# Kernel tuning notes

Measured on AMD Instinct MI355X. Metric: run time of the kernel, lower is better.

The kernel has to match this reference:

```python
import jax, jax.numpy as jnp
import numpy as np

B, S, D, H = 4, 2048, 1024, 4096
EPS = 1e-5

def _layernorm(x, g, b):
    mu = jnp.mean(x, axis=-1, keepdims=True)
    var = jnp.mean(jnp.square(x - mu), axis=-1, keepdims=True)
    return (x - mu) * jax.lax.rsqrt(var + EPS) * g + b

def setup_inputs() -> dict:
    key = jax.random.key(0)
    ks = jax.random.split(key, 8)
    s = lambda d: 1.0 / np.sqrt(d)
    return {
        "x": jax.random.normal(ks[0], (B, S, D), jnp.float32),
        "Wq": jax.random.normal(ks[1], (D, D), jnp.float32) * s(D),
        "bq": jnp.zeros((D,), jnp.float32),
        "Wk": jax.random.normal(ks[2], (D, D), jnp.float32) * s(D),
        "bk": jnp.zeros((D,), jnp.float32),
        "Wv": jax.random.normal(ks[3], (D, D), jnp.float32) * s(D),
        "bv": jnp.zeros((D,), jnp.float32),
        "Wo": jax.random.normal(ks[4], (D, D), jnp.float32) * s(D),
        "bo": jnp.zeros((D,), jnp.float32),
        "g1": jnp.ones((D,), jnp.float32),
        "be1": jnp.zeros((D,), jnp.float32),
        "g2": jnp.ones((D,), jnp.float32),
        "be2": jnp.zeros((D,), jnp.float32),
        "W1": jax.random.normal(ks[5], (D, H), jnp.float32) * s(D),
        "b1": jnp.zeros((H,), jnp.float32),
        "W2": jax.random.normal(ks[6], (H, D), jnp.float32) * s(H),
        "b2": jnp.zeros((D,), jnp.float32),
    }

def reference(x, Wq, bq, Wk, bk, Wv, bv, Wo, bo, g1, be1, g2, be2, W1, b1, W2, b2):
    # pre-norm self-attention + residual
    xn = _layernorm(x, g1, be1)
    q = xn @ Wq + bq            # [B,S,D]
    k = xn @ Wk + bk
    v = xn @ Wv + bv
    scale = 1.0 / jnp.sqrt(jnp.float32(D))
    scores = jnp.einsum("bsd,btd->bst", q, k) * scale  # [B,S,S]
    attn = jax.nn.softmax(scores, axis=-1)
    attn_out = jnp.einsum("bst,btd->bsd", attn, v) @ Wo + bo
    x = x + attn_out
    # pre-norm MLP + residual
    xn2 = _layernorm(x, g2, be2)
    ffn = jax.nn.relu(xn2 @ W1 + b1) @ W2 + b2
    out = x + ffn
    return out, attn
```

## Files before the change

kernel.cpp:

```cpp
#include <hip/hip_runtime.h>
#include <hip/hip_bf16.h>


typedef __bf16 bf16_t;
typedef __bf16 bf16x8 __attribute__((ext_vector_type(8)));
typedef float  f32x4  __attribute__((ext_vector_type(4)));

#define EPI_QKV            0
#define EPI_BF16_SCALE     1
#define EPI_BF16           3
#define EPI_F32_BIAS_RES   4
#define EPI_BF16_RELU_BIAS 5

__device__ __forceinline__ void gl_lds16(const bf16_t* g, void* l) {
  __builtin_amdgcn_global_load_lds(
      (const __attribute__((address_space(1))) void*)g,
      (__attribute__((address_space(3))) void*)l, 16, 0, 0);
}

template<int BM, int EPI>
__global__ __launch_bounds__(512, 2)
void gemm8p(const bf16_t* __restrict__ A, const bf16_t* __restrict__ B,
            float* __restrict__ Cf, bf16_t* __restrict__ Cb,
            const float* __restrict__ bias,
            int M, int N, int K, long sAb, long sBb, long sCb, float scale)
{
  constexpr int BN  = 256;
  constexpr int WTM = BM / 2;
  constexpr int MF  = WTM / 16;
  constexpr int NF  = 4;
  constexpr int LA  = BM / 128;
  constexpr int LB  = 2;
  constexpr int L   = LA + LB;
  constexpr int L0  = 2;
  constexpr int SBUF = (BM + BN) * 64;
  constexpr int W   = 2 * L;
  __shared__ __align__(16) char lds[4 * SBUF];

  const int tid = threadIdx.x;
  const int l   = tid & 63;
  const int w   = tid >> 6;
  const int wm  = w >> 2;
  const int wn  = w & 3;

  const int nx = gridDim.x, ny = gridDim.y;
  const int tot = nx * ny * gridDim.z;
  int id = blockIdx.x + nx * (blockIdx.y + ny * blockIdx.z);
  const int cpx = tot >> 3;
  int s = (id & 7) * cpx + (id >> 3);
  const int bx = s % nx; int rq = s / nx;
  const int by = rq % ny; const int bz = rq / ny;

  const bf16_t* Ab = A + (long)bz * sAb;
  const bf16_t* Bb = B + (long)bz * sBb;
  const int m0 = by * BM, n0 = bx * BN;
  const int NT = K >> 5;

  const int srow = w * 16 + (l >> 2);
  const int scol = ((l & 3) ^ ((l >> 3) & 3)) * 8;
  const bf16_t* srcA[LA]; const bf16_t* srcB[LB];
#pragma unroll
  for (int q = 0; q < LA; ++q) srcA[q] = Ab + (long)(m0 + q * 128 + srow) * K + scol;
#pragma unroll
  for (int q = 0; q < LB; ++q) srcB[q] = Bb + (long)(n0 + q * 128 + srow) * K + scol;
  const int ldsA = w * 1024;
  const int ldsB = BM * 64 + w * 1024;

  const int rA0 = wm * WTM + (l & 15);
  const int rB0 = wn * 64 + (l & 15);
  const int xoff = 16 * ((l >> 4) ^ ((l >> 1) & 3));

  f32x4 acc[MF][NF] = {};
  bf16x8 afr[MF / 2], bfr[NF];

#pragma unroll
  for (int d = 0; d < 3; ++d) {
    char* bufS = lds + d * SBUF;
    const long kst = (long)d * 32;
#pragma unroll
    for (int q = 0; q < LA; ++q) gl_lds16(srcA[q] + kst, bufS + ldsA + q * 8192);
#pragma unroll
    for (int q = 0; q < LB; ++q) gl_lds16(srcB[q] + kst, bufS + ldsB + q * 8192);
  }
  asm volatile("s_waitcnt vmcnt(%0)" :: "n"(W) : "memory");
  __builtin_amdgcn_s_barrier();
  __builtin_amdgcn_sched_barrier(0);

  for (int t = 0; t < NT; ++t) {
    const char* bufR = lds + (t & 3) * SBUF;
    char* bufS = lds + ((t + 3) & 3) * SBUF;
    const int tst = t + 3;
    const long kst = (long)((tst < NT) ? tst : (NT - 1)) * 32;

#pragma unroll
    for (int nf = 0; nf < NF; ++nf)
      bfr[nf] = *(const bf16x8*)(bufR + BM * 64 + (rB0 + nf * 16) * 64 + xoff);
#pragma unroll
    for (int mf = 0; mf < MF / 2; ++mf)
      afr[mf] = *(const bf16x8*)(bufR + (rA0 + mf * 16) * 64 + xoff);
#pragma unroll
    for (int q = 0; q < L0; ++q) {
      if (q < LA) gl_lds16(srcA[q] + kst, bufS + ldsA + q * 8192);
      else        gl_lds16(srcB[q - LA] + kst, bufS + ldsB + (q - LA) * 8192);
    }
    __builtin_amdgcn_s_barrier();
    __builtin_amdgcn_s_setprio(1);
#pragma unroll
    for (int mf = 0; mf < MF / 2; ++mf)
#pragma unroll
      for (int nf = 0; nf < NF; ++nf)
        acc[mf][nf] = __builtin_amdgcn_mfma_f32_16x16x32_bf16(afr[mf], bfr[nf], acc[mf][nf], 0, 0, 0);
    __builtin_amdgcn_s_setprio(0);
    __builtin_amdgcn_s_barrier();

#pragma unroll
    for (int mf = 0; mf < MF / 2; ++mf)
      afr[mf] = *(const bf16x8*)(bufR + (rA0 + (MF / 2 + mf) * 16) * 64 + xoff);
#pragma unroll
    for (int q = L0; q < L; ++q) {
      if (q < LA) gl_lds16(srcA[q] + kst, bufS + ldsA + q * 8192);
      else        gl_lds16(srcB[q - LA] + kst, bufS + ldsB + (q - LA) * 8192);
    }
    __builtin_amdgcn_s_barrier();
    __builtin_amdgcn_s_setprio(1);
#pragma unroll
    for (int mf = 0; mf < MF / 2; ++mf)
#pragma unroll
      for (int nf = 0; nf < NF; ++nf)
        acc[MF / 2 + mf][nf] = __builtin_amdgcn_mfma_f32_16x16x32_bf16(afr[mf], bfr[nf], acc[MF / 2 + mf][nf], 0, 0, 0);
    __builtin_amdgcn_s_setprio(0);
    asm volatile("s_waitcnt vmcnt(%0)" :: "n"(W) : "memory");
    __builtin_amdgcn_s_barrier();
    __builtin_amdgcn_sched_barrier(0);
  }
  asm volatile("s_waitcnt vmcnt(0)" ::: "memory");

  const int colB0 = n0 + wn * 64 + (l & 15);
  const int rowB0 = m0 + wm * WTM + ((l >> 4) << 2);
#pragma unroll
  for (int mi = 0; mi < MF; ++mi) {
#pragma unroll
    for (int ni = 0; ni < NF; ++ni) {
      const int col = colB0 + ni * 16;
#pragma unroll
      for (int j = 0; j < 4; ++j) {
        const int row = rowB0 + mi * 16 + j;
        const float v = acc[mi][ni][j];
        if constexpr (EPI == EPI_BF16_SCALE) {
          Cb[sCb * bz + (long)row * N + col] = (bf16_t)(v * scale);
        } else {
          const float u = v + bias[col];
          Cb[(long)row * N + col] = (bf16_t)(u > 0.f ? u : 0.f);
        }
      }
    }
  }
}

template<int EPI>
__global__ __launch_bounds__(512, 1)
void gemm128(const bf16_t* __restrict__ A, const bf16_t* __restrict__ B,
             float* __restrict__ Cf, bf16_t* __restrict__ Cb,
             const float* __restrict__ bias, const float* __restrict__ resid,
             int M, int N, int K, long sAb, long sBb, long sCb)
{
  constexpr int SBUF = 49152;
  __shared__ __align__(16) char lds[3 * SBUF];
  const int tid = threadIdx.x;
  const int l   = tid & 63;
  const int w   = tid >> 6;
  const int wm  = w >> 2, wn = w & 3;

  const int nx = gridDim.x, ny = gridDim.y;
  const int tot = nx * ny * gridDim.z;
  int id = blockIdx.x + nx * (blockIdx.y + ny * blockIdx.z);
  const int cpx = tot >> 3;
  int sid = (id & 7) * cpx + (id >> 3);
  const int bx = sid % nx; int rq = sid / nx;
  const int by = rq % ny; const int bz = rq / ny;

  const bf16_t* Ab = A + (long)bz * sAb;
  const bf16_t* Bb = B + (long)bz * sBb;
  const int m0 = by * 128, n0 = bx * 256;
  const int NT = K >> 6;

  const int scol = ((l & 7) ^ (l >> 3)) * 8;
  const bf16_t* srcA = Ab + (long)(m0 + 16 * w + (l >> 3)) * K + scol;
  const bf16_t* srcB = Bb + (long)(n0 + 32 * w + (l >> 3)) * K + scol;
  const int dA = w * 2048 + l * 16;
  const int dB = 16384 + w * 4096 + l * 16;

  const int rA = wm * 64 + (l & 15);
  const int rB = wn * 64 + (l & 15);
  const int xo = ((l >> 4) ^ (l & 7)) * 16;
  const int aoff = rA * 128 + xo;
  const int boff = 16384 + rB * 128 + xo;

  f32x4 acc[4][4] = {};
  bf16x8 af[4], bv[4];

  {
    char* b0 = lds; char* b1 = lds + SBUF;
#pragma unroll
    for (int q = 0; q < 2; ++q) gl_lds16(srcA + (long)q * 8 * K, b0 + dA + q * 1024);
#pragma unroll
    for (int q = 0; q < 4; ++q) gl_lds16(srcB + (long)q * 8 * K, b0 + dB + q * 1024);
#pragma unroll
    for (int q = 0; q < 2; ++q) gl_lds16(srcA + (long)q * 8 * K + 64, b1 + dA + q * 1024);
#pragma unroll
    for (int q = 0; q < 4; ++q) gl_lds16(srcB + (long)q * 8 * K + 64, b1 + dB + q * 1024);
  }
  asm volatile("s_waitcnt vmcnt(6)" ::: "memory");
  __builtin_amdgcn_s_barrier();
  __builtin_amdgcn_sched_barrier(0);

  int ir = 0, is = 2;
  for (int t = 0; t < NT; ++t) {
    const char* bufR = lds + ir * SBUF;
    char* bufS = lds + is * SBUF;
    const int tst = (t + 2 < NT) ? t + 2 : NT - 1;
    const long kst = (long)tst * 64;

#pragma unroll
    for (int nf = 0; nf < 4; ++nf) bv[nf] = *(const bf16x8*)(bufR + boff + nf * 2048);
#pragma unroll
    for (int mf = 0; mf < 4; ++mf) af[mf] = *(const bf16x8*)(bufR + aoff + mf * 2048);
    gl_lds16(srcA + kst,                 bufS + dA);
    gl_lds16(srcA + (long)8 * K + kst,   bufS + dA + 1024);
    gl_lds16(srcB + kst,                 bufS + dB);
    __builtin_amdgcn_s_barrier();
    __builtin_amdgcn_s_setprio(1);
#pragma unroll
    for (int mf = 0; mf < 4; ++mf)
#pragma unroll
      for (int nf = 0; nf < 4; ++nf)
        acc[mf][nf] = __builtin_amdgcn_mfma_f32_16x16x32_bf16(af[mf], bv[nf], acc[mf][nf], 0, 0, 0);
    __builtin_amdgcn_s_setprio(0);
    __builtin_amdgcn_s_barrier();

#pragma unroll
    for (int nf = 0; nf < 4; ++nf) bv[nf] = *(const bf16x8*)(bufR + ((boff + nf * 2048) ^ 64));
#pragma unroll
    for (int mf = 0; mf < 4; ++mf) af[mf] = *(const bf16x8*)(bufR + ((aoff + mf * 2048) ^ 64));
    gl_lds16(srcB + (long)8 * K + kst,   bufS + dB + 1024);
    gl_lds16(srcB + (long)16 * K + kst,  bufS + dB + 2048);
    gl_lds16(srcB + (long)24 * K + kst,  bufS + dB + 3072);
    __builtin_amdgcn_s_barrier();
    __builtin_amdgcn_s_setprio(1);
#pragma unroll
    for (int mf = 0; mf < 4; ++mf)
#pragma unroll
      for (int nf = 0; nf < 4; ++nf)
        acc[mf][nf] = __builtin_amdgcn_mfma_f32_16x16x32_bf16(af[mf], bv[nf], acc[mf][nf], 0, 0, 0);
    __builtin_amdgcn_s_setprio(0);
    asm volatile("s_waitcnt vmcnt(6)" ::: "memory");
    __builtin_amdgcn_s_barrier();
    __builtin_amdgcn_sched_barrier(0);
    ir = (ir == 2) ? 0 : ir + 1;
    is = (is == 2) ? 0 : is + 1;
  }
  asm volatile("s_waitcnt vmcnt(0)" ::: "memory");

  const int colB0 = n0 + wn * 64 + (l & 15);
  const int rowB0 = m0 + wm * 64 + ((l >> 4) << 2);
#pragma unroll
  for (int mi = 0; mi < 4; ++mi) {
#pragma unroll
    for (int ni = 0; ni < 4; ++ni) {
      const int col = colB0 + ni * 16;
#pragma unroll
      for (int j = 0; j < 4; ++j) {
        const int row = rowB0 + mi * 16 + j;
        const float v = acc[mi][ni][j];
        if constexpr (EPI == EPI_BF16) {
          Cb[sCb * bz + (long)row * N + col] = (bf16_t)v;
        } else {
          Cf[(long)row * N + col] = v + bias[col] + resid[(long)row * N + col];
        }
      }
    }
  }
}

__global__ __launch_bounds__(512, 3)
void gemm128_32(const bf16_t* __restrict__ A, const bf16_t* __restrict__ B,
                bf16_t* __restrict__ Cb, bf16_t* __restrict__ Cb2,
                bf16_t* __restrict__ Cb3,
                const float* __restrict__ bias, const float* __restrict__ bias2,
                const float* __restrict__ bias3, int M, int N, int K)
{
  constexpr int SBUF = 24576;
  __shared__ __align__(16) char lds[2 * SBUF];
  const int tid = threadIdx.x;
  const int l   = tid & 63;
  const int w   = tid >> 6;
  const int wm  = w >> 2, wn = w & 3;

  const int nx = gridDim.x, ny = gridDim.y;
  const int tot = nx * ny;
  int id = blockIdx.x + nx * blockIdx.y;
  const int cpx = tot >> 3;
  int sid = (id & 7) * cpx + (id >> 3);
  const int bx = sid % nx;
  const int by = sid / nx;

  const int m0 = by * 128, n0 = bx * 256;
  const int NT = K >> 5;

  const int srow = (l >> 2);
  const int scol = ((l & 3) ^ ((l >> 3) & 3)) * 8;
  const bf16_t* srcA = A + (long)(m0 + w * 16 + srow) * K + scol;
  const bf16_t* srcB0 = B + (long)(n0 + w * 32 + srow) * K + scol;
  const bf16_t* srcB1 = srcB0 + (long)16 * K;
  const int dA = w * 1024 + l * 16;
  const int dB = 8192 + w * 2048 + l * 16;

  const int rA = wm * 64 + (l & 15);
  const int rB = wn * 64 + (l & 15);
  const int xoff = 16 * ((l >> 4) ^ ((l >> 1) & 3));
  const int aoff = rA * 64 + xoff;
  const int boff = 8192 + rB * 64 + xoff;

  f32x4 acc[4][4] = {};
  bf16x8 af[4], bv[4];

  gl_lds16(srcA, lds + dA);
  gl_lds16(srcB0, lds + dB);
  gl_lds16(srcB1, lds + dB + 1024);
  asm volatile("s_waitcnt vmcnt(0)" ::: "memory");
  __builtin_amdgcn_s_barrier();
  __builtin_amdgcn_sched_barrier(0);

  for (int t = 0; t < NT; ++t) {
    const char* bufR = lds + (t & 1) * SBUF;
    char* bufS = lds + ((t + 1) & 1) * SBUF;
    const long kst = (long)((t + 1 < NT) ? t + 1 : NT - 1) * 32;

#pragma unroll
    for (int nf = 0; nf < 4; ++nf) bv[nf] = *(const bf16x8*)(bufR + boff + nf * 1024);
#pragma unroll
    for (int mf = 0; mf < 4; ++mf) af[mf] = *(const bf16x8*)(bufR + aoff + mf * 1024);
    gl_lds16(srcA + kst, bufS + dA);
    gl_lds16(srcB0 + kst, bufS + dB);
    gl_lds16(srcB1 + kst, bufS + dB + 1024);
    __builtin_amdgcn_s_setprio(1);
#pragma unroll
    for (int mf = 0; mf < 4; ++mf)
#pragma unroll
      for (int nf = 0; nf < 4; ++nf)
        acc[mf][nf] = __builtin_amdgcn_mfma_f32_16x16x32_bf16(af[mf], bv[nf], acc[mf][nf], 0, 0, 0);
    __builtin_amdgcn_s_setprio(0);
    asm volatile("s_waitcnt vmcnt(0)" ::: "memory");
    __builtin_amdgcn_s_barrier();
    __builtin_amdgcn_sched_barrier(0);
  }

  const int colB0 = n0 + wn * 64 + (l & 15);
  const int rowB0 = m0 + wm * 64 + ((l >> 4) << 2);
#pragma unroll
  for (int mi = 0; mi < 4; ++mi) {
#pragma unroll
    for (int ni = 0; ni < 4; ++ni) {
      const int col = colB0 + ni * 16;
#pragma unroll
      for (int j = 0; j < 4; ++j) {
        const int row = rowB0 + mi * 16 + j;
        const float v = acc[mi][ni][j];
        if (col < 1024)      Cb [(long)row * 1024 + col]        = (bf16_t)(v + bias[col]);
        else if (col < 2048) Cb2[(long)row * 1024 + col - 1024] = (bf16_t)(v + bias2[col - 1024]);
        else                 Cb3[(long)row * 1024 + col - 2048] = (bf16_t)(v + bias3[col - 2048]);
      }
    }
  }
}

__global__ __launch_bounds__(256)
void transpose_bf(const bf16_t* __restrict__ V, bf16_t* __restrict__ VT)
{
  __shared__ __align__(16) bf16_t t[64][72];
  const int b = blockIdx.z;
  const int t0 = blockIdx.y * 64, d0 = blockIdx.x * 64;
  const int r = threadIdx.x >> 3;
  const int c = (threadIdx.x & 7) * 8;
  const bf16_t* src = V + ((long)b * 2048 + t0) * 1024 + d0;
#pragma unroll
  for (int h = 0; h < 2; ++h)
    *(bf16x8*)&t[r + 32 * h][c] = *(const bf16x8*)(src + (long)(r + 32 * h) * 1024 + c);
  __syncthreads();
  bf16_t* dst = VT + ((long)b * 1024 + d0) * 2048 + t0;
#pragma unroll
  for (int h = 0; h < 2; ++h) {
    const int d = r + 32 * h;
    bf16x8 o;
#pragma unroll
    for (int j = 0; j < 8; ++j) o[j] = t[c + j][d];
    *(bf16x8*)(dst + (long)d * 2048 + c) = o;
  }
}

__global__ __launch_bounds__(256)
void transpose_all(const float* __restrict__ Wq, const float* __restrict__ Wk,
                   const float* __restrict__ Wv, const float* __restrict__ Wo,
                   const float* __restrict__ W1, const float* __restrict__ W2,
                   bf16_t* __restrict__ WqkvT, bf16_t* __restrict__ WoT,
                   bf16_t* __restrict__ W1T, bf16_t* __restrict__ W2T)
{
  const int id = blockIdx.x;
  const float* W; bf16_t* WT; int R, C, cb, rb;
  if (id < 4096) {
    const int wsel = id >> 10, loc = id & 1023;
    cb = loc & 31; rb = loc >> 5; R = 1024; C = 1024;
    if (wsel == 0)      { W = Wq; WT = WqkvT; }
    else if (wsel == 1) { W = Wk; WT = WqkvT + 1024L * 1024; }
    else if (wsel == 2) { W = Wv; WT = WqkvT + 2048L * 1024; }
    else                { W = Wo; WT = WoT; }
  } else if (id < 8192) {
    const int loc = id - 4096;
    cb = loc & 127; rb = loc >> 7; R = 1024; C = 4096;
    W = W1; WT = W1T;
  } else {
    const int loc = id - 8192;
    cb = loc & 31; rb = loc >> 5; R = 4096; C = 1024;
    W = W2; WT = W2T;
  }
  __shared__ float t[32][33];
  const int c0 = cb * 32, r0 = rb * 32;
  const int tx = threadIdx.x & 31, ty = threadIdx.x >> 5;
#pragma unroll
  for (int i = 0; i < 32; i += 8)
    t[ty + i][tx] = W[(long)(r0 + ty + i) * C + c0 + tx];
  __syncthreads();
#pragma unroll
  for (int i = 0; i < 32; i += 8)
    WT[(long)(c0 + ty + i) * R + r0 + tx] = (bf16_t)t[tx][ty + i];
}

__global__ __launch_bounds__(256)
void ln_kernel(const float* __restrict__ x, const float* __restrict__ g,
               const float* __restrict__ be, bf16_t* __restrict__ out)
{
  const long row = blockIdx.x;
  const float4 v = *(const float4*)(x + row * 1024 + threadIdx.x * 4);
  float s  = v.x + v.y + v.z + v.w;
  float s2 = v.x * v.x + v.y * v.y + v.z * v.z + v.w * v.w;
  __shared__ float red[10];
  const int lane = threadIdx.x & 63, w = threadIdx.x >> 6;
#pragma unroll
  for (int off = 32; off; off >>= 1) {
    s  += __shfl_down(s, off);
    s2 += __shfl_down(s2, off);
  }
  if (lane == 0) { red[w] = s; red[4 + w] = s2; }
  __syncthreads();
  if (threadIdx.x == 0) {
    const float ts = red[0] + red[1] + red[2] + red[3];
    const float t2 = red[4] + red[5] + red[6] + red[7];
    const float mu = ts * (1.f / 1024.f);
    const float var = t2 * (1.f / 1024.f) - mu * mu;
    red[8] = mu;
    red[9] = rsqrtf(var + 1e-5f);
  }
  __syncthreads();
  const float mu = red[8], rinv = red[9];
  const int c = threadIdx.x * 4;
  const float4 gv = *(const float4*)(g + c);
  const float4 bvv = *(const float4*)(be + c);
  bf16_t* o = out + row * 1024 + c;
  o[0] = (bf16_t)((v.x - mu) * rinv * gv.x + bvv.x);
  o[1] = (bf16_t)((v.y - mu) * rinv * gv.y + bvv.y);
  o[2] = (bf16_t)((v.z - mu) * rinv * gv.z + bvv.z);
  o[3] = (bf16_t)((v.w - mu) * rinv * gv.w + bvv.w);
}

__global__ __launch_bounds__(256)
void softmax_kernel(float* __restrict__ sc, bf16_t* __restrict__ ab)
{
  const long row = blockIdx.x;
  const int t0 = threadIdx.x * 8;
  const bf16x8 v8 = *(const bf16x8*)(ab + row * 2048 + t0);
  float e[8];
#pragma unroll
  for (int j = 0; j < 8; ++j) e[j] = (float)v8[j];
  float mx = fmaxf(fmaxf(fmaxf(e[0], e[1]), fmaxf(e[2], e[3])),
                   fmaxf(fmaxf(e[4], e[5]), fmaxf(e[6], e[7])));
  __shared__ float red[4];
  __shared__ float bc[2];
  const int lane = threadIdx.x & 63, w = threadIdx.x >> 6;
#pragma unroll
  for (int off = 32; off; off >>= 1) mx = fmaxf(mx, __shfl_down(mx, off));
  if (lane == 0) red[w] = mx;
  __syncthreads();
  if (threadIdx.x == 0) bc[0] = fmaxf(fmaxf(red[0], red[1]), fmaxf(red[2], red[3]));
  __syncthreads();
  const float m = bc[0];
  float s = 0.f;
#pragma unroll
  for (int j = 0; j < 8; ++j) { e[j] = __expf(e[j] - m); s += e[j]; }
#pragma unroll
  for (int off = 32; off; off >>= 1) s += __shfl_down(s, off);
  __syncthreads();
  if (lane == 0) red[w] = s;
  __syncthreads();
  if (threadIdx.x == 0) bc[1] = 1.f / (red[0] + red[1] + red[2] + red[3]);
  __syncthreads();
  const float inv = bc[1];
  float4 oa, ob;
  oa.x = e[0] * inv; oa.y = e[1] * inv; oa.z = e[2] * inv; oa.w = e[3] * inv;
  ob.x = e[4] * inv; ob.y = e[5] * inv; ob.z = e[6] * inv; ob.w = e[7] * inv;
  *(float4*)(sc + row * 2048 + t0)     = oa;
  *(float4*)(sc + row * 2048 + t0 + 4) = ob;
  bf16x8 o8;
  o8[0] = (bf16_t)oa.x; o8[1] = (bf16_t)oa.y; o8[2] = (bf16_t)oa.z; o8[3] = (bf16_t)oa.w;
  o8[4] = (bf16_t)ob.x; o8[5] = (bf16_t)ob.y; o8[6] = (bf16_t)ob.z; o8[7] = (bf16_t)ob.w;
  *(bf16x8*)(ab + row * 2048 + t0) = o8;
}

extern "C" void kernel_launch(void* const* d_in, const int* in_sizes, int n_in,
                              void* d_out, int out_size, void* d_ws, size_t ws_size,
                              hipStream_t stream)
{
  const float* x   = (const float*)d_in[0];
  const float* Wq  = (const float*)d_in[1];
  const float* bq  = (const float*)d_in[2];
  const float* Wk  = (const float*)d_in[3];
  const float* bk  = (const float*)d_in[4];
  const float* Wv  = (const float*)d_in[5];
  const float* bv  = (const float*)d_in[6];
  const float* Wo  = (const float*)d_in[7];
  const float* bo  = (const float*)d_in[8];
  const float* g1  = (const float*)d_in[9];
  const float* be1 = (const float*)d_in[10];
  const float* g2  = (const float*)d_in[11];
  const float* be2 = (const float*)d_in[12];
  const float* W1  = (const float*)d_in[13];
  const float* b1  = (const float*)d_in[14];
  const float* W2  = (const float*)d_in[15];
  const float* b2  = (const float*)d_in[16];

  float* out   = (float*)d_out;
  float* attnF = out + 8192L * 1024;
  bf16_t* vB   = (bf16_t*)attnF;

  char* ws = (char*)d_ws;
  const size_t MB = 1024 * 1024;
  bf16_t* WqkvT = (bf16_t*)(ws + 0 * MB);
  bf16_t* WoT   = (bf16_t*)(ws + 6 * MB);
  bf16_t* W1T   = (bf16_t*)(ws + 8 * MB);
  bf16_t* W2T   = (bf16_t*)(ws + 16 * MB);
  bf16_t* xn    = (bf16_t*)(ws + 24 * MB);
  bf16_t* qB    = (bf16_t*)(ws + 40 * MB);
  bf16_t* kB    = (bf16_t*)(ws + 56 * MB);
  bf16_t* vT    = (bf16_t*)(ws + 72 * MB);
  bf16_t* atB   = (bf16_t*)(ws + 88 * MB);
  float*  x2    = (float* )(ws + 120 * MB);
  bf16_t* hB    = (bf16_t*)(ws + 56 * MB);

  transpose_all<<<12288, 256, 0, stream>>>(
      Wq, Wk, Wv, Wo, W1, W2, WqkvT, WoT, W1T, W2T);

  ln_kernel<<<8192, 256, 0, stream>>>(x, g1, be1, xn);

  gemm128_32<<<dim3(12, 64), 512, 0, stream>>>(
      xn, WqkvT, qB, kB, vB, bq, bk, bv, 8192, 3072, 1024);

  transpose_bf<<<dim3(16, 32, 4), 256, 0, stream>>>(vB, vT);

  gemm8p<256, EPI_BF16_SCALE><<<dim3(8, 8, 4), 512, 0, stream>>>(
      qB, kB, nullptr, atB, nullptr,
      2048, 2048, 1024, 2048L * 1024, 2048L * 1024, 2048L * 2048, 0.03125f);

  softmax_kernel<<<8192, 256, 0, stream>>>(attnF, atB);

  gemm128<EPI_BF16><<<dim3(4, 16, 4), 512, 0, stream>>>(
      atB, vT, nullptr, qB, nullptr, nullptr,
      2048, 1024, 2048, 2048L * 2048, 1024L * 2048, 2048L * 1024);

  gemm128<EPI_F32_BIAS_RES><<<dim3(4, 64, 1), 512, 0, stream>>>(
      qB, WoT, x2, nullptr, bo, x,
      8192, 1024, 1024, 0, 0, 0);

  ln_kernel<<<8192, 256, 0, stream>>>(x2, g2, be2, xn);

  gemm8p<256, EPI_BF16_RELU_BIAS><<<dim3(16, 32, 1), 512, 0, stream>>>(
      xn, W1T, nullptr, hB, b1,
      8192, 4096, 1024, 0, 0, 0, 1.f);
  gemm128<EPI_F32_BIAS_RES><<<dim3(4, 64, 1), 512, 0, stream>>>(
      hB, W2T, out, nullptr, b2, x2,
      8192, 1024, 4096, 0, 0, 0);
}
```

Before: 390.2 us.

## Enlarge QKV GEMM tile to 256x256 with split-phase staged loads

Replaces the 128x256 QKV projection GEMM with a 256x256 tile kernel, where each wave computes 128x64 of output using 8x4 accumulators. The K-step is split into two halves: A loads are issued before the first MFMA block and B loads before the second, with barriers between them. The larger tile cuts global loads per FLOP and halves the grid to 384 blocks. In exchange it raises register pressure (occupancy drops to 2 blocks), adds barriers, and leaves fewer blocks to fill the CUs.

```diff
diff --git a/kernel.cpp b/kernel.cpp
--- a/kernel.cpp
+++ b/kernel.cpp
@@ -282,14 +282,14 @@
   }
 }
 
-__global__ __launch_bounds__(512, 3)
-void gemm128_32(const bf16_t* __restrict__ A, const bf16_t* __restrict__ B,
-                bf16_t* __restrict__ Cb, bf16_t* __restrict__ Cb2,
-                bf16_t* __restrict__ Cb3,
-                const float* __restrict__ bias, const float* __restrict__ bias2,
-                const float* __restrict__ bias3, int M, int N, int K)
-{
-  constexpr int SBUF = 24576;
+__global__ __launch_bounds__(512, 2)
+void gemm256q(const bf16_t* __restrict__ A, const bf16_t* __restrict__ B,
+              bf16_t* __restrict__ Cb, bf16_t* __restrict__ Cb2,
+              bf16_t* __restrict__ Cb3,
+              const float* __restrict__ bias, const float* __restrict__ bias2,
+              const float* __restrict__ bias3, int M, int N, int K)
+{
+  constexpr int SBUF = 32768;
   __shared__ __align__(16) char lds[2 * SBUF];
   const int tid = threadIdx.x;
   const int l   = tid & 63;
@@ -304,29 +304,29 @@
   const int bx = sid % nx;
   const int by = sid / nx;
 
-  const int m0 = by * 128, n0 = bx * 256;
+  const int m0 = by * 256, n0 = bx * 256;
   const int NT = K >> 5;
 
-  const int srow = (l >> 2);
+  const int srow = w * 16 + (l >> 2);
   const int scol = ((l & 3) ^ ((l >> 3) & 3)) * 8;
-  const bf16_t* srcA = A + (long)(m0 + w * 16 + srow) * K + scol;
-  const bf16_t* srcB0 = B + (long)(n0 + w * 32 + srow) * K + scol;
-  const bf16_t* srcB1 = srcB0 + (long)16 * K;
-  const int dA = w * 1024 + l * 16;
-  const int dB = 8192 + w * 2048 + l * 16;
-
-  const int rA = wm * 64 + (l & 15);
-  const int rB = wn * 64 + (l & 15);
+  const bf16_t* srcA0 = A + (long)(m0 + srow) * K + scol;
+  const bf16_t* srcA1 = A + (long)(m0 + 128 + srow) * K + scol;
+  const bf16_t* srcB0 = B + (long)(n0 + srow) * K + scol;
+  const bf16_t* srcB1 = B + (long)(n0 + 128 + srow) * K + scol;
+  const int ldsA = w * 1024;
+  const int ldsB = 16384 + w * 1024;
+
+  const int rA0 = wm * 128 + (l & 15);
+  const int rB0 = wn * 64 + (l & 15);
   const int xoff = 16 * ((l >> 4) ^ ((l >> 1) & 3));
-  const int aoff = rA * 64 + xoff;
-  const int boff = 8192 + rB * 64 + xoff;
-
-  f32x4 acc[4][4] = {};
-  bf16x8 af[4], bv[4];
-
-  gl_lds16(srcA, lds + dA);
-  gl_lds16(srcB0, lds + dB);
-  gl_lds16(srcB1, lds + dB + 1024);
+
+  f32x4 acc[8][4] = {};
+  bf16x8 afr[4], bfr[4];
+
+  gl_lds16(srcA0, lds + ldsA);
+  gl_lds16(srcA1, lds + ldsA + 8192);
+  gl_lds16(srcB0, lds + ldsB);
+  gl_lds16(srcB1, lds + ldsB + 8192);
   asm volatile("s_waitcnt vmcnt(0)" ::: "memory");
   __builtin_amdgcn_s_barrier();
   __builtin_amdgcn_sched_barrier(0);
@@ -337,18 +337,35 @@
     const long kst = (long)((t + 1 < NT) ? t + 1 : NT - 1) * 32;
 
 #pragma unroll
-    for (int nf = 0; nf < 4; ++nf) bv[nf] = *(const bf16x8*)(bufR + boff + nf * 1024);
-#pragma unroll
-    for (int mf = 0; mf < 4; ++mf) af[mf] = *(const bf16x8*)(bufR + aoff + mf * 1024);
-    gl_lds16(srcA + kst, bufS + dA);
-    gl_lds16(srcB0 + kst, bufS + dB);
-    gl_lds16(srcB1 + kst, bufS + dB + 1024);
+    for (int nf = 0; nf < 4; ++nf)
+      bfr[nf] = *(const bf16x8*)(bufR + 16384 + (rB0 + nf * 16) * 64 + xoff);
+#pragma unroll
+    for (int mf = 0; mf < 4; ++mf)
+      afr[mf] = *(const bf16x8*)(bufR + (rA0 + mf * 16) * 64 + xoff);
+    gl_lds16(srcA0 + kst, bufS + ldsA);
+    gl_lds16(srcA1 + kst, bufS + ldsA + 8192);
+    __builtin_amdgcn_s_barrier();
     __builtin_amdgcn_s_setprio(1);
 #pragma unroll
     for (int mf = 0; mf < 4; ++mf)
 #pragma unroll
       for (int nf = 0; nf < 4; ++nf)
-        acc[mf][nf] = __builtin_amdgcn_mfma_f32_16x16x32_bf16(af[mf], bv[nf], acc[mf][nf], 0, 0, 0);
+        acc[mf][nf] = __builtin_amdgcn_mfma_f32_16x16x32_bf16(afr[mf], bfr[nf], acc[mf][nf], 0, 0, 0);
+    __builtin_amdgcn_s_setprio(0);
+    __builtin_amdgcn_s_barrier();
+
+#pragma unroll
+    for (int mf = 0; mf < 4; ++mf)
+      afr[mf] = *(const bf16x8*)(bufR + (rA0 + (4 + mf) * 16) * 64 + xoff);
+    gl_lds16(srcB0 + kst, bufS + ldsB);
+    gl_lds16(srcB1 + kst, bufS + ldsB + 8192);
+    __builtin_amdgcn_s_barrier();
+    __builtin_amdgcn_s_setprio(1);
+#pragma unroll
+    for (int mf = 0; mf < 4; ++mf)
+#pragma unroll
+      for (int nf = 0; nf < 4; ++nf)
+        acc[4 + mf][nf] = __builtin_amdgcn_mfma_f32_16x16x32_bf16(afr[mf], bfr[nf], acc[4 + mf][nf], 0, 0, 0);
     __builtin_amdgcn_s_setprio(0);
     asm volatile("s_waitcnt vmcnt(0)" ::: "memory");
     __builtin_amdgcn_s_barrier();
@@ -356,9 +373,9 @@
   }
 
   const int colB0 = n0 + wn * 64 + (l & 15);
-  const int rowB0 = m0 + wm * 64 + ((l >> 4) << 2);
-#pragma unroll
-  for (int mi = 0; mi < 4; ++mi) {
+  const int rowB0 = m0 + wm * 128 + ((l >> 4) << 2);
+#pragma unroll
+  for (int mi = 0; mi < 8; ++mi) {
 #pragma unroll
     for (int ni = 0; ni < 4; ++ni) {
       const int col = colB0 + ni * 16;
@@ -560,7 +577,7 @@
 
   ln_kernel<<<8192, 256, 0, stream>>>(x, g1, be1, xn);
 
-  gemm128_32<<<dim3(12, 64), 512, 0, stream>>>(
+  gemm256q<<<dim3(12, 32), 512, 0, stream>>>(
       xn, WqkvT, qB, kB, vB, bq, bk, bv, 8192, 3072, 1024);
 
   transpose_bf<<<dim3(16, 32, 4), 256, 0, stream>>>(vB, vT);
```

After: 412.8 us. +5.8%, slower.
